# Kernel tuning notes

Measured on AMD Instinct MI355X. Metric: run time of the kernel, lower is better.

The kernel has to match this reference:

```python
import jax, jax.numpy as jnp
import numpy as np

E = 400000
N = 100000
B = 64
D = 128          # token_dim
H = 128          # hidden_dim
A = 2 * H        # action_dim


def setup_inputs() -> dict:
    key = jax.random.key(0)
    ks = jax.random.split(key, 12)
    inp = {
        "relation_tokens": jax.random.normal(ks[0], (E, D), jnp.float32),
        "node_tokens": jax.random.normal(ks[1], (N, D), jnp.float32),
        "edge_index": jax.random.randint(ks[2], (2, E), 0, N, jnp.int64 if jax.config.jax_enable_x64 else jnp.int32),
        "question_tokens": jax.random.normal(ks[3], (B, D), jnp.float32),
        "edge_batch": jax.random.randint(ks[4], (E,), 0, B, jnp.int64 if jax.config.jax_enable_x64 else jnp.int32),
        # learned params (xavier-like small init); stored as [in, out] for x @ W
        "W_rel": jax.random.normal(ks[5], (D, H), jnp.float32) * 0.05,
        "W_node": jax.random.normal(ks[6], (D, H), jnp.float32) * 0.05,
        "W_qgate": jax.random.normal(ks[7], (D, A), jnp.float32) * 0.05,
        "W_mlp1": jax.random.normal(ks[8], (A, A), jnp.float32) * 0.05,
        "b_mlp1": jnp.zeros((A,), jnp.float32),
        "W_mlp2": jax.random.normal(ks[9], (A, A), jnp.float32) * 0.05,
        "b_mlp2": jnp.zeros((A,), jnp.float32),
    }
    return inp


def reference(relation_tokens, node_tokens, edge_index, question_tokens, edge_batch,
              W_rel, W_node, W_qgate, W_mlp1, b_mlp1, W_mlp2, b_mlp2):
    # TrajectoryAgent.precompute_action_keys (dropout=0 -> identity)
    tail_nodes = edge_index[1]                       # [E]
    tail_tokens = node_tokens[tail_nodes]            # gather -> [E, D]
    q_tokens = question_tokens[edge_batch]           # gather -> [E, D]

    rel_key = relation_tokens @ W_rel                # [E, H]
    node_key = tail_tokens @ W_node                  # [E, H]
    q_gate = jax.nn.sigmoid(q_tokens @ W_qgate)      # [E, 2H]

    action_key = jnp.concatenate((rel_key, node_key), axis=-1) * q_gate  # [E, 2H]

    # action_mlp: Linear -> exact GELU -> Linear (torch nn.GELU default = erf)
    h = jax.nn.gelu(action_key @ W_mlp1 + b_mlp1, approximate=False)
    return h @ W_mlp2 + b_mlp2                       # [E, 2H]
```

## Files before the change

### kernel.cpp

```cpp
#include <hip/hip_runtime.h>

typedef __bf16 bf16;
typedef bf16 bf16x4 __attribute__((ext_vector_type(4)));
typedef bf16 bf16x8 __attribute__((ext_vector_type(8)));
typedef float f32x4 __attribute__((ext_vector_type(4)));

#define WS_PK1   0
#define WS_PK2   32768
#define WS_PK3   98304
#define WS_QG    163840

__global__ void prep_weights(const float* __restrict__ Wrel,
                             const float* __restrict__ Wnode,
                             const float* __restrict__ W1,
                             const float* __restrict__ W2,
                             bf16* __restrict__ ws) {
  int id = blockIdx.x * 256 + threadIdx.x;
  if (id < 32768) {
    int cg = id >> 13, rem = id & 8191;
    int kk = rem >> 11;
    int ai = (rem >> 9) & 3;
    int l  = (rem >> 3) & 63;
    int j  = rem & 7;
    int n  = (cg & 1) * 64 + ai * 16 + (l & 15);
    int k  = kk * 32 + (l >> 4) * 8 + j;
    const float* src = (cg >> 1) ? Wnode : Wrel;
    ws[WS_PK1 + id] = (bf16)src[k * 128 + n];
  } else if (id < 98304) {
    int t = id - 32768;
    int cg = t >> 14, rem = t & 16383;
    int kk = rem >> 11;
    int ai = (rem >> 9) & 3;
    int l  = (rem >> 3) & 63;
    int j  = rem & 7;
    int n  = cg * 64 + ai * 16 + (l & 15);
    int k  = kk * 32 + (l >> 4) * 8 + j;
    ws[WS_PK2 + t] = (bf16)W1[k * 256 + n];
  } else if (id < 163840) {
    int t = id - 98304;
    int cg = t >> 14, rem = t & 16383;
    int kk = rem >> 11;
    int ai = (rem >> 9) & 3;
    int l  = (rem >> 3) & 63;
    int j  = rem & 7;
    int n  = cg * 64 + ai * 16 + (l & 15);
    int k  = kk * 32 + (l >> 4) * 8 + j;
    ws[WS_PK3 + t] = (bf16)W2[k * 256 + n];
  }
}

__global__ void prep_qg(const float* __restrict__ question,
                        const float* __restrict__ Wq,
                        bf16* __restrict__ qg) {
  int b = blockIdx.x, c = threadIdx.x;
  float s = 0.f;
#pragma unroll 8
  for (int k = 0; k < 128; ++k) s += question[b * 128 + k] * Wq[k * 256 + c];
  qg[b * 256 + c] = (bf16)(1.f / (1.f + expf(-s)));
}

__device__ __forceinline__ float gelu_fast(float x) {
  float x2 = x * x;
  float p = fmaf(0.0356774081f, x2, 0.7978845608f);
  float y = p * x;
  float e = __expf(2.f * y);
  float r = __builtin_amdgcn_rcpf(e + 1.f);
  float th = 1.f - 2.f * r;
  return 0.5f * x * (1.f + th);
}

typedef __attribute__((address_space(1))) const void gq_t;
typedef __attribute__((address_space(3))) void lq_t;
#define GLD16(g, s) __builtin_amdgcn_global_load_lds((gq_t*)(g), (lq_t*)(s), 16, 0, 0)
#define SB() __builtin_amdgcn_sched_barrier(0xF)
#define WAIT_VM4()   { asm volatile("s_waitcnt vmcnt(4)" ::: "memory"); SB(); }
#define WAIT_VM0()   { asm volatile("s_waitcnt vmcnt(0)" ::: "memory"); SB(); }
#define WAIT_LGKM0() { asm volatile("s_waitcnt lgkmcnt(0)" ::: "memory"); SB(); }
#define BAR() __builtin_amdgcn_s_barrier()

__global__ __launch_bounds__(256, 2) void fused_main(
    const float* __restrict__ rel_tok,
    const float* __restrict__ node_tok,
    const int*   __restrict__ tail_idx,
    const int*   __restrict__ ebatch,
    const bf16*  __restrict__ pk1,
    const bf16*  __restrict__ pk2,
    const bf16*  __restrict__ pk3,
    const bf16*  __restrict__ qg,
    const float* __restrict__ b1,
    const float* __restrict__ b2,
    float* __restrict__ out)
{
  __shared__ char  s_buf[32768];
  __shared__ char  s_w[32768];
  __shared__ float s_bias[512];

  const int tid = threadIdx.x;
  const int cg  = tid >> 6;
  const int l   = tid & 63;
  const int lo  = l & 15;
  const int hi  = l >> 4;
  const int base = blockIdx.x * 64;
  const int h1  = cg >> 1;

  auto issue_step = [&](int s) {
    const bf16* g;
    if (s < 4)       g = pk1 + cg * 8192  + s * 2048;
    else if (s < 12) g = pk2 + cg * 16384 + (s - 4) * 2048;
    else             g = pk3 + cg * 16384 + (s - 12) * 2048;
    g += l * 8;
    char* d = s_w + (s & 1) * 16384 + cg * 4096;
#pragma unroll
    for (int ai = 0; ai < 4; ++ai) GLD16(g + ai * 512, d + ai * 1024);
  };

  int ebv[4];
#pragma unroll
  for (int bj = 0; bj < 4; ++bj) ebv[bj] = ebatch[base + bj * 16 + lo];
  bf16x4 gv[4][4];
#pragma unroll
  for (int bj = 0; bj < 4; ++bj)
#pragma unroll
    for (int ai = 0; ai < 4; ++ai)
      gv[bj][ai] = *(const bf16x4*)(qg + ebv[bj] * 256 + cg * 64 + ai * 16 + hi * 4);
  s_bias[tid]       = b1[tid];
  s_bias[256 + tid] = b2[tid];

  {
    const float4* g = (const float4*)rel_tok + (size_t)base * 32;
#pragma unroll
    for (int i = 0; i < 8; ++i) {
      int idx = tid + i * 256;
      int row = idx >> 5, c4 = idx & 31;
      float4 v = g[idx];
      bf16x4 b; b[0] = (bf16)v.x; b[1] = (bf16)v.y; b[2] = (bf16)v.z; b[3] = (bf16)v.w;
      int off = row * 256 + ((c4 * 8) ^ ((row & 15) << 4));
      *(bf16x4*)(s_buf + off) = b;
    }
#pragma unroll
    for (int i = 0; i < 8; ++i) {
      int idx = tid + i * 256;
      int row = idx >> 5, c4 = idx & 31;
      int tail = tail_idx[base + row];
      float4 v = ((const float4*)node_tok)[(size_t)tail * 32 + c4];
      bf16x4 b; b[0] = (bf16)v.x; b[1] = (bf16)v.y; b[2] = (bf16)v.z; b[3] = (bf16)v.w;
      int off = 16384 + row * 256 + ((c4 * 8) ^ ((row & 15) << 4));
      *(bf16x4*)(s_buf + off) = b;
    }
  }

  WAIT_VM0();
  issue_step(0);
  issue_step(1);
  WAIT_LGKM0();
  BAR();

  const f32x4 zero4 = {0.f, 0.f, 0.f, 0.f};
  const int wb = cg * 4096 + l * 16;

  f32x4 acc1[4][4];
#pragma unroll
  for (int ai = 0; ai < 4; ++ai)
#pragma unroll
    for (int bj = 0; bj < 4; ++bj) acc1[ai][bj] = zero4;

#pragma unroll
  for (int kk = 0; kk < 4; ++kk) {
    const int s = kk;
    WAIT_VM4();
    bf16x8 a[4];
#pragma unroll
    for (int ai = 0; ai < 4; ++ai)
      a[ai] = *(const bf16x8*)(s_w + (s & 1) * 16384 + wb + ai * 1024);
    WAIT_LGKM0();
    issue_step(s + 2);
    __builtin_amdgcn_s_setprio(1);
#pragma unroll
    for (int bj = 0; bj < 4; ++bj) {
      int e = bj * 16 + lo;
      bf16x8 b = *(const bf16x8*)(s_buf + h1 * 16384 + e * 256 +
                                  ((kk * 64 + hi * 16) ^ ((e & 15) << 4)));
#pragma unroll
      for (int ai = 0; ai < 4; ++ai)
        acc1[ai][bj] = __builtin_amdgcn_mfma_f32_16x16x32_bf16(a[ai], b, acc1[ai][bj], 0, 0, 0);
    }
    __builtin_amdgcn_s_setprio(0);
  }
  BAR();

#pragma unroll
  for (int bj = 0; bj < 4; ++bj) {
    int e = bj * 16 + lo;
#pragma unroll
    for (int ai = 0; ai < 4; ++ai) {
      int col0 = cg * 64 + ai * 16 + hi * 4;
      bf16x4 pk;
      pk[0] = (bf16)(acc1[ai][bj][0] * (float)gv[bj][ai][0]);
      pk[1] = (bf16)(acc1[ai][bj][1] * (float)gv[bj][ai][1]);
      pk[2] = (bf16)(acc1[ai][bj][2] * (float)gv[bj][ai][2]);
      pk[3] = (bf16)(acc1[ai][bj][3] * (float)gv[bj][ai][3]);
      int off = e * 512 + ((2 * col0) ^ ((e & 15) << 4));
      *(bf16x4*)(s_buf + off) = pk;
    }
  }
  WAIT_LGKM0();
  BAR();

  f32x4 acc2[4][4];
#pragma unroll
  for (int ai = 0; ai < 4; ++ai)
#pragma unroll
    for (int bj = 0; bj < 4; ++bj) acc2[ai][bj] = zero4;

#pragma unroll
  for (int kk = 0; kk < 8; ++kk) {
    const int s = 4 + kk;
    WAIT_VM4();
    bf16x8 a[4];
#pragma unroll
    for (int ai = 0; ai < 4; ++ai)
      a[ai] = *(const bf16x8*)(s_w + (s & 1) * 16384 + wb + ai * 1024);
    WAIT_LGKM0();
    issue_step(s + 2);
    __builtin_amdgcn_s_setprio(1);
#pragma unroll
    for (int bj = 0; bj < 4; ++bj) {
      int e = bj * 16 + lo;
      bf16x8 b = *(const bf16x8*)(s_buf + e * 512 +
                                  ((kk * 64 + hi * 16) ^ ((e & 15) << 4)));
#pragma unroll
      for (int ai = 0; ai < 4; ++ai)
        acc2[ai][bj] = __builtin_amdgcn_mfma_f32_16x16x32_bf16(a[ai], b, acc2[ai][bj], 0, 0, 0);
    }
    __builtin_amdgcn_s_setprio(0);
  }
  BAR();

#pragma unroll
  for (int bj = 0; bj < 4; ++bj) {
    int e = bj * 16 + lo;
#pragma unroll
    for (int ai = 0; ai < 4; ++ai) {
      int col0 = cg * 64 + ai * 16 + hi * 4;
      float4 bv = *(const float4*)(s_bias + col0);
      bf16x4 pk;
      pk[0] = (bf16)gelu_fast(acc2[ai][bj][0] + bv.x);
      pk[1] = (bf16)gelu_fast(acc2[ai][bj][1] + bv.y);
      pk[2] = (bf16)gelu_fast(acc2[ai][bj][2] + bv.z);
      pk[3] = (bf16)gelu_fast(acc2[ai][bj][3] + bv.w);
      int off = e * 512 + ((2 * col0) ^ ((e & 15) << 4));
      *(bf16x4*)(s_buf + off) = pk;
    }
  }
  WAIT_LGKM0();
  BAR();

  f32x4 acc3[4][4];
#pragma unroll
  for (int ai = 0; ai < 4; ++ai)
#pragma unroll
    for (int bj = 0; bj < 4; ++bj) acc3[ai][bj] = zero4;

#pragma unroll
  for (int kk = 0; kk < 8; ++kk) {
    const int s = 12 + kk;
    if (s < 19) { WAIT_VM4(); } else { WAIT_VM0(); }
    bf16x8 a[4];
#pragma unroll
    for (int ai = 0; ai < 4; ++ai)
      a[ai] = *(const bf16x8*)(s_w + (s & 1) * 16384 + wb + ai * 1024);
    WAIT_LGKM0();
    if (s + 2 <= 19) issue_step(s + 2);
    __builtin_amdgcn_s_setprio(1);
#pragma unroll
    for (int bj = 0; bj < 4; ++bj) {
      int e = bj * 16 + lo;
      bf16x8 b = *(const bf16x8*)(s_buf + e * 512 +
                                  ((kk * 64 + hi * 16) ^ ((e & 15) << 4)));
#pragma unroll
      for (int ai = 0; ai < 4; ++ai)
        acc3[ai][bj] = __builtin_amdgcn_mfma_f32_16x16x32_bf16(a[ai], b, acc3[ai][bj], 0, 0, 0);
    }
    __builtin_amdgcn_s_setprio(0);
  }

#pragma unroll
  for (int bj = 0; bj < 4; ++bj) {
    int e = bj * 16 + lo;
#pragma unroll
    for (int ai = 0; ai < 4; ++ai) {
      int col0 = cg * 64 + ai * 16 + hi * 4;
      float4 bv = *(const float4*)(s_bias + 256 + col0);
      float4 o;
      o.x = acc3[ai][bj][0] + bv.x;
      o.y = acc3[ai][bj][1] + bv.y;
      o.z = acc3[ai][bj][2] + bv.z;
      o.w = acc3[ai][bj][3] + bv.w;
      *(float4*)(out + (size_t)(base + e) * 256 + col0) = o;
    }
  }
}

extern "C" void kernel_launch(void* const* d_in, const int* in_sizes, int n_in,
                              void* d_out, int out_size, void* d_ws, size_t ws_size,
                              hipStream_t stream) {
  const float* rel    = (const float*)d_in[0];
  const float* node   = (const float*)d_in[1];
  const int*   eidx   = (const int*)d_in[2];
  const float* quest  = (const float*)d_in[3];
  const int*   ebat   = (const int*)d_in[4];
  const float* Wrel   = (const float*)d_in[5];
  const float* Wnode  = (const float*)d_in[6];
  const float* Wq     = (const float*)d_in[7];
  const float* W1     = (const float*)d_in[8];
  const float* bias1  = (const float*)d_in[9];
  const float* W2     = (const float*)d_in[10];
  const float* bias2  = (const float*)d_in[11];
  float* outp = (float*)d_out;
  bf16* ws = (bf16*)d_ws;

  const int E = in_sizes[4];

  prep_weights<<<640, 256, 0, stream>>>(Wrel, Wnode, W1, W2, ws);
  prep_qg<<<64, 256, 0, stream>>>(quest, Wq, ws + WS_QG);
  fused_main<<<E / 64, 256, 0, stream>>>(
      rel, node, eidx + E, ebat,
      ws + WS_PK1, ws + WS_PK2, ws + WS_PK3, ws + WS_QG,
      bias1, bias2, outp);
}
```

Before: 281.8 us.

## Stream weights through a 4-slot sub-step LDS ring to fit three blocks per CU

Weight tiles are now fetched in 4KB sub-steps into a 4-slot LDS ring with three loads in flight, instead of two 16KB double-buffered steps. Waits move to per-sub-step vmcnt checks, and the B operand fragments are loaded once per k-step before the per-ai MFMA groups. This halves the weight LDS buffer, so launch bounds can request three blocks per CU, aiming for more latency hiding and occupancy. The cost is finer-grained waits and more issue overhead per sub-step. Register pressure under the tighter launch bound may also cause spills.

```diff
diff --git a/kernel.cpp b/kernel.cpp
--- a/kernel.cpp
+++ b/kernel.cpp
@@ -72,13 +72,17 @@
 typedef __attribute__((address_space(1))) const void gq_t;
 typedef __attribute__((address_space(3))) void lq_t;
 #define GLD16(g, s) __builtin_amdgcn_global_load_lds((gq_t*)(g), (lq_t*)(s), 16, 0, 0)
-#define SB() __builtin_amdgcn_sched_barrier(0xF)
-#define WAIT_VM4()   { asm volatile("s_waitcnt vmcnt(4)" ::: "memory"); SB(); }
-#define WAIT_VM0()   { asm volatile("s_waitcnt vmcnt(0)" ::: "memory"); SB(); }
-#define WAIT_LGKM0() { asm volatile("s_waitcnt lgkmcnt(0)" ::: "memory"); SB(); }
+#define SBF() __builtin_amdgcn_sched_barrier(0xF)
+#define SB7() __builtin_amdgcn_sched_barrier(0x7)
+#define WAIT_VM0()   { asm volatile("s_waitcnt vmcnt(0)" ::: "memory"); SBF(); }
+#define WAIT_LGKM0() { asm volatile("s_waitcnt lgkmcnt(0)" ::: "memory"); SBF(); }
+#define VMWAIT(u)    { if ((u) <= 77)      { asm volatile("s_waitcnt vmcnt(2)" ::: "memory"); } \
+                       else if ((u) == 78) { asm volatile("s_waitcnt vmcnt(1)" ::: "memory"); } \
+                       else                { asm volatile("s_waitcnt vmcnt(0)" ::: "memory"); } \
+                       SBF(); }
 #define BAR() __builtin_amdgcn_s_barrier()
 
-__global__ __launch_bounds__(256, 2) void fused_main(
+__global__ __launch_bounds__(256, 3) void fused_main(
     const float* __restrict__ rel_tok,
     const float* __restrict__ node_tok,
     const int*   __restrict__ tail_idx,
@@ -92,7 +96,7 @@
     float* __restrict__ out)
 {
   __shared__ char  s_buf[32768];
-  __shared__ char  s_w[32768];
+  __shared__ char  s_w[16384];
   __shared__ float s_bias[512];
 
   const int tid = threadIdx.x;
@@ -103,15 +107,12 @@
   const int base = blockIdx.x * 64;
   const int h1  = cg >> 1;
 
-  auto issue_step = [&](int s) {
+  auto issue_sub = [&](int u) {
     const bf16* g;
-    if (s < 4)       g = pk1 + cg * 8192  + s * 2048;
-    else if (s < 12) g = pk2 + cg * 16384 + (s - 4) * 2048;
-    else             g = pk3 + cg * 16384 + (s - 12) * 2048;
-    g += l * 8;
-    char* d = s_w + (s & 1) * 16384 + cg * 4096;
-#pragma unroll
-    for (int ai = 0; ai < 4; ++ai) GLD16(g + ai * 512, d + ai * 1024);
+    if (u < 16)      g = pk1 + cg * 8192  + u * 512;
+    else if (u < 48) g = pk2 + cg * 16384 + (u - 16) * 512;
+    else             g = pk3 + cg * 16384 + (u - 48) * 512;
+    GLD16(g + l * 8, s_w + (u & 3) * 4096 + cg * 1024 + l * 16);
   };
 
   int ebv[4];
@@ -150,13 +151,14 @@
   }
 
   WAIT_VM0();
-  issue_step(0);
-  issue_step(1);
+  issue_sub(0);
+  issue_sub(1);
+  issue_sub(2);
   WAIT_LGKM0();
   BAR();
 
   const f32x4 zero4 = {0.f, 0.f, 0.f, 0.f};
-  const int wb = cg * 4096 + l * 16;
+  const int wrd = cg * 1024 + l * 16;
 
   f32x4 acc1[4][4];
 #pragma unroll
@@ -166,25 +168,26 @@
 
 #pragma unroll
   for (int kk = 0; kk < 4; ++kk) {
-    const int s = kk;
-    WAIT_VM4();
-    bf16x8 a[4];
-#pragma unroll
-    for (int ai = 0; ai < 4; ++ai)
-      a[ai] = *(const bf16x8*)(s_w + (s & 1) * 16384 + wb + ai * 1024);
-    WAIT_LGKM0();
-    issue_step(s + 2);
-    __builtin_amdgcn_s_setprio(1);
+    bf16x8 bf[4];
 #pragma unroll
     for (int bj = 0; bj < 4; ++bj) {
       int e = bj * 16 + lo;
-      bf16x8 b = *(const bf16x8*)(s_buf + h1 * 16384 + e * 256 +
-                                  ((kk * 64 + hi * 16) ^ ((e & 15) << 4)));
-#pragma unroll
-      for (int ai = 0; ai < 4; ++ai)
-        acc1[ai][bj] = __builtin_amdgcn_mfma_f32_16x16x32_bf16(a[ai], b, acc1[ai][bj], 0, 0, 0);
-    }
-    __builtin_amdgcn_s_setprio(0);
+      bf[bj] = *(const bf16x8*)(s_buf + h1 * 16384 + e * 256 +
+                                ((kk * 64 + hi * 16) ^ ((e & 15) << 4)));
+    }
+#pragma unroll
+    for (int ai = 0; ai < 4; ++ai) {
+      const int u = kk * 4 + ai;
+      VMWAIT(u);
+      bf16x8 a = *(const bf16x8*)(s_w + (u & 3) * 4096 + wrd);
+      __builtin_amdgcn_s_setprio(1);
+#pragma unroll
+      for (int bj = 0; bj < 4; ++bj)
+        acc1[ai][bj] = __builtin_amdgcn_mfma_f32_16x16x32_bf16(a, bf[bj], acc1[ai][bj], 0, 0, 0);
+      __builtin_amdgcn_s_setprio(0);
+      SB7();
+      issue_sub(u + 3);
+    }
   }
   BAR();
 
@@ -214,25 +217,26 @@
 
 #pragma unroll
   for (int kk = 0; kk < 8; ++kk) {
-    const int s = 4 + kk;
-    WAIT_VM4();
-    bf16x8 a[4];
-#pragma unroll
-    for (int ai = 0; ai < 4; ++ai)
-      a[ai] = *(const bf16x8*)(s_w + (s & 1) * 16384 + wb + ai * 1024);
-    WAIT_LGKM0();
-    issue_step(s + 2);
-    __builtin_amdgcn_s_setprio(1);
+    bf16x8 bf[4];
 #pragma unroll
     for (int bj = 0; bj < 4; ++bj) {
       int e = bj * 16 + lo;
-      bf16x8 b = *(const bf16x8*)(s_buf + e * 512 +
-                                  ((kk * 64 + hi * 16) ^ ((e & 15) << 4)));
-#pragma unroll
-      for (int ai = 0; ai < 4; ++ai)
-        acc2[ai][bj] = __builtin_amdgcn_mfma_f32_16x16x32_bf16(a[ai], b, acc2[ai][bj], 0, 0, 0);
-    }
-    __builtin_amdgcn_s_setprio(0);
+      bf[bj] = *(const bf16x8*)(s_buf + e * 512 +
+                                ((kk * 64 + hi * 16) ^ ((e & 15) << 4)));
+    }
+#pragma unroll
+    for (int ai = 0; ai < 4; ++ai) {
+      const int u = 16 + kk * 4 + ai;
+      VMWAIT(u);
+      bf16x8 a = *(const bf16x8*)(s_w + (u & 3) * 4096 + wrd);
+      __builtin_amdgcn_s_setprio(1);
+#pragma unroll
+      for (int bj = 0; bj < 4; ++bj)
+        acc2[ai][bj] = __builtin_amdgcn_mfma_f32_16x16x32_bf16(a, bf[bj], acc2[ai][bj], 0, 0, 0);
+      __builtin_amdgcn_s_setprio(0);
+      SB7();
+      issue_sub(u + 3);
+    }
   }
   BAR();
 
@@ -263,25 +267,25 @@
 
 #pragma unroll
   for (int kk = 0; kk < 8; ++kk) {
-    const int s = 12 + kk;
-    if (s < 19) { WAIT_VM4(); } else { WAIT_VM0(); }
-    bf16x8 a[4];
-#pragma unroll
-    for (int ai = 0; ai < 4; ++ai)
-      a[ai] = *(const bf16x8*)(s_w + (s & 1) * 16384 + wb + ai * 1024);
-    WAIT_LGKM0();
-    if (s + 2 <= 19) issue_step(s + 2);
-    __builtin_amdgcn_s_setprio(1);
+    bf16x8 bf[4];
 #pragma unroll
     for (int bj = 0; bj < 4; ++bj) {
       int e = bj * 16 + lo;
-      bf16x8 b = *(const bf16x8*)(s_buf + e * 512 +
-                                  ((kk * 64 + hi * 16) ^ ((e & 15) << 4)));
-#pragma unroll
-      for (int ai = 0; ai < 4; ++ai)
-        acc3[ai][bj] = __builtin_amdgcn_mfma_f32_16x16x32_bf16(a[ai], b, acc3[ai][bj], 0, 0, 0);
-    }
-    __builtin_amdgcn_s_setprio(0);
+      bf[bj] = *(const bf16x8*)(s_buf + e * 512 +
+                                ((kk * 64 + hi * 16) ^ ((e & 15) << 4)));
+    }
+#pragma unroll
+    for (int ai = 0; ai < 4; ++ai) {
+      const int u = 48 + kk * 4 + ai;
+      VMWAIT(u);
+      bf16x8 a = *(const bf16x8*)(s_w + (u & 3) * 4096 + wrd);
+      __builtin_amdgcn_s_setprio(1);
+#pragma unroll
+      for (int bj = 0; bj < 4; ++bj)
+        acc3[ai][bj] = __builtin_amdgcn_mfma_f32_16x16x32_bf16(a, bf[bj], acc3[ai][bj], 0, 0, 0);
+      __builtin_amdgcn_s_setprio(0);
+      if (u + 3 < 80) { SB7(); issue_sub(u + 3); }
+    }
   }
 
 #pragma unroll
```

Measured after the change: 285.4 us. No clear change (+1.3%).

## Make fused kernel persistent and prefetch next tile's inputs during GEMMs

Applied to the files above, without the earlier changes.

The fused kernel now runs as a persistent grid of 512 blocks, each looping over 64-edge tiles with a stride of the grid size. Tail indices and batch ids for the next tile are loaded during the first GEMM. Relation rows, gathered node rows and q-gate values are loaded into registers during the last GEMM and written to LDS after the output store. This hides the input-gather latency behind MFMA work and removes per-block launch and prologue cost, at the price of more register pressure (rv/nv/gv2 arrays), which could spill or hurt occupancy at 2 blocks per CU.

```diff
diff --git a/kernel.cpp b/kernel.cpp
--- a/kernel.cpp
+++ b/kernel.cpp
@@ -72,10 +72,9 @@
 typedef __attribute__((address_space(1))) const void gq_t;
 typedef __attribute__((address_space(3))) void lq_t;
 #define GLD16(g, s) __builtin_amdgcn_global_load_lds((gq_t*)(g), (lq_t*)(s), 16, 0, 0)
-#define SB() __builtin_amdgcn_sched_barrier(0xF)
-#define WAIT_VM4()   { asm volatile("s_waitcnt vmcnt(4)" ::: "memory"); SB(); }
-#define WAIT_VM0()   { asm volatile("s_waitcnt vmcnt(0)" ::: "memory"); SB(); }
-#define WAIT_LGKM0() { asm volatile("s_waitcnt lgkmcnt(0)" ::: "memory"); SB(); }
+#define SBF() __builtin_amdgcn_sched_barrier(0xF)
+#define WAIT_VM(n)   { asm volatile("s_waitcnt vmcnt(" #n ")" ::: "memory"); SBF(); }
+#define WAIT_LGKM0() { asm volatile("s_waitcnt lgkmcnt(0)" ::: "memory"); SBF(); }
 #define BAR() __builtin_amdgcn_s_barrier()
 
 __global__ __launch_bounds__(256, 2) void fused_main(
@@ -89,7 +88,8 @@
     const bf16*  __restrict__ qg,
     const float* __restrict__ b1,
     const float* __restrict__ b2,
-    float* __restrict__ out)
+    float* __restrict__ out,
+    int ntiles, int G)
 {
   __shared__ char  s_buf[32768];
   __shared__ char  s_w[32768];
@@ -100,8 +100,8 @@
   const int l   = tid & 63;
   const int lo  = l & 15;
   const int hi  = l >> 4;
-  const int base = blockIdx.x * 64;
   const int h1  = cg >> 1;
+  const int c4s = tid & 31;
 
   auto issue_step = [&](int s) {
     const bf16* g;
@@ -114,190 +114,241 @@
     for (int ai = 0; ai < 4; ++ai) GLD16(g + ai * 512, d + ai * 1024);
   };
 
-  int ebv[4];
-#pragma unroll
-  for (int bj = 0; bj < 4; ++bj) ebv[bj] = ebatch[base + bj * 16 + lo];
-  bf16x4 gv[4][4];
-#pragma unroll
-  for (int bj = 0; bj < 4; ++bj)
-#pragma unroll
-    for (int ai = 0; ai < 4; ++ai)
-      gv[bj][ai] = *(const bf16x4*)(qg + ebv[bj] * 256 + cg * 64 + ai * 16 + hi * 4);
   s_bias[tid]       = b1[tid];
   s_bias[256 + tid] = b2[tid];
 
+  const int t0 = blockIdx.x;
+  bf16x4 gv[4][4];
   {
-    const float4* g = (const float4*)rel_tok + (size_t)base * 32;
+    int ebv[4];
+#pragma unroll
+    for (int bj = 0; bj < 4; ++bj) ebv[bj] = ebatch[t0 * 64 + bj * 16 + lo];
+#pragma unroll
+    for (int bj = 0; bj < 4; ++bj)
+#pragma unroll
+      for (int ai = 0; ai < 4; ++ai)
+        gv[bj][ai] = *(const bf16x4*)(qg + ebv[bj] * 256 + cg * 64 + ai * 16 + hi * 4);
+    const float4* g = (const float4*)rel_tok + (size_t)t0 * 2048;
 #pragma unroll
     for (int i = 0; i < 8; ++i) {
-      int idx = tid + i * 256;
-      int row = idx >> 5, c4 = idx & 31;
-      float4 v = g[idx];
+      int row = (tid >> 5) + 8 * i;
+      float4 v = g[tid + i * 256];
       bf16x4 b; b[0] = (bf16)v.x; b[1] = (bf16)v.y; b[2] = (bf16)v.z; b[3] = (bf16)v.w;
-      int off = row * 256 + ((c4 * 8) ^ ((row & 15) << 4));
+      int off = row * 256 + ((c4s * 8) ^ ((row & 15) << 4));
       *(bf16x4*)(s_buf + off) = b;
     }
 #pragma unroll
     for (int i = 0; i < 8; ++i) {
-      int idx = tid + i * 256;
-      int row = idx >> 5, c4 = idx & 31;
-      int tail = tail_idx[base + row];
-      float4 v = ((const float4*)node_tok)[(size_t)tail * 32 + c4];
+      int row = (tid >> 5) + 8 * i;
+      int tail = tail_idx[t0 * 64 + row];
+      float4 v = ((const float4*)node_tok)[(size_t)tail * 32 + c4s];
       bf16x4 b; b[0] = (bf16)v.x; b[1] = (bf16)v.y; b[2] = (bf16)v.z; b[3] = (bf16)v.w;
-      int off = 16384 + row * 256 + ((c4 * 8) ^ ((row & 15) << 4));
+      int off = 16384 + row * 256 + ((c4s * 8) ^ ((row & 15) << 4));
       *(bf16x4*)(s_buf + off) = b;
     }
   }
 
-  WAIT_VM0();
-  issue_step(0);
-  issue_step(1);
-  WAIT_LGKM0();
-  BAR();
-
   const f32x4 zero4 = {0.f, 0.f, 0.f, 0.f};
-  const int wb = cg * 4096 + l * 16;
-
-  f32x4 acc1[4][4];
-#pragma unroll
-  for (int ai = 0; ai < 4; ++ai)
-#pragma unroll
-    for (int bj = 0; bj < 4; ++bj) acc1[ai][bj] = zero4;
-
-#pragma unroll
-  for (int kk = 0; kk < 4; ++kk) {
-    const int s = kk;
-    WAIT_VM4();
-    bf16x8 a[4];
+  const int wrd = cg * 4096 + l * 16;
+
+  for (int t = t0; t < ntiles; t += G) {
+    const int base = t * 64;
+    int tn = t + G; if (tn >= ntiles) tn = t;
+
+    WAIT_VM(0);
+    issue_step(0);
+    issue_step(1);
+    WAIT_LGKM0();
+    BAR();
+
+    int t2l[8], eb2v[4];
+    bf16x4 gv2[4][4];
+
+    f32x4 acc1[4][4];
 #pragma unroll
     for (int ai = 0; ai < 4; ++ai)
-      a[ai] = *(const bf16x8*)(s_w + (s & 1) * 16384 + wb + ai * 1024);
-    WAIT_LGKM0();
-    issue_step(s + 2);
-    __builtin_amdgcn_s_setprio(1);
+#pragma unroll
+      for (int bj = 0; bj < 4; ++bj) acc1[ai][bj] = zero4;
+
+#pragma unroll
+    for (int kk = 0; kk < 4; ++kk) {
+      if (kk == 0)      { WAIT_VM(4); }
+      else if (kk < 3)  { WAIT_VM(16); }
+      else              { WAIT_VM(4); }
+      bf16x8 a[4];
+#pragma unroll
+      for (int ai = 0; ai < 4; ++ai)
+        a[ai] = *(const bf16x8*)(s_w + (kk & 1) * 16384 + wrd + ai * 1024);
+      WAIT_LGKM0();
+      issue_step(kk + 2);
+      if (kk == 0) {
+        SBF();
+#pragma unroll
+        for (int i = 0; i < 8; ++i) t2l[i] = tail_idx[tn * 64 + (tid >> 5) + 8 * i];
+#pragma unroll
+        for (int bj = 0; bj < 4; ++bj) eb2v[bj] = ebatch[tn * 64 + bj * 16 + lo];
+        SBF();
+      }
+      __builtin_amdgcn_s_setprio(1);
+#pragma unroll
+      for (int bj = 0; bj < 4; ++bj) {
+        int e = bj * 16 + lo;
+        bf16x8 b = *(const bf16x8*)(s_buf + h1 * 16384 + e * 256 +
+                                    ((kk * 64 + hi * 16) ^ ((e & 15) << 4)));
+#pragma unroll
+        for (int ai = 0; ai < 4; ++ai)
+          acc1[ai][bj] = __builtin_amdgcn_mfma_f32_16x16x32_bf16(a[ai], b, acc1[ai][bj], 0, 0, 0);
+      }
+      __builtin_amdgcn_s_setprio(0);
+    }
+    BAR();
+
 #pragma unroll
     for (int bj = 0; bj < 4; ++bj) {
       int e = bj * 16 + lo;
-      bf16x8 b = *(const bf16x8*)(s_buf + h1 * 16384 + e * 256 +
-                                  ((kk * 64 + hi * 16) ^ ((e & 15) << 4)));
+#pragma unroll
+      for (int ai = 0; ai < 4; ++ai) {
+        int col0 = cg * 64 + ai * 16 + hi * 4;
+        bf16x4 pk;
+        pk[0] = (bf16)(acc1[ai][bj][0] * (float)gv[bj][ai][0]);
+        pk[1] = (bf16)(acc1[ai][bj][1] * (float)gv[bj][ai][1]);
+        pk[2] = (bf16)(acc1[ai][bj][2] * (float)gv[bj][ai][2]);
+        pk[3] = (bf16)(acc1[ai][bj][3] * (float)gv[bj][ai][3]);
+        int off = e * 512 + ((2 * col0) ^ ((e & 15) << 4));
+        *(bf16x4*)(s_buf + off) = pk;
+      }
+    }
+    WAIT_LGKM0();
+    BAR();
+
+    f32x4 acc2[4][4];
+#pragma unroll
+    for (int ai = 0; ai < 4; ++ai)
+#pragma unroll
+      for (int bj = 0; bj < 4; ++bj) acc2[ai][bj] = zero4;
+
+#pragma unroll
+    for (int kk = 0; kk < 8; ++kk) {
+      const int s = 4 + kk;
+      WAIT_VM(4);
+      bf16x8 a[4];
 #pragma unroll
       for (int ai = 0; ai < 4; ++ai)
-        acc1[ai][bj] = __builtin_amdgcn_mfma_f32_16x16x32_bf16(a[ai], b, acc1[ai][bj], 0, 0, 0);
-    }
-    __builtin_amdgcn_s_setprio(0);
-  }
-  BAR();
-
-#pragma unroll
-  for (int bj = 0; bj < 4; ++bj) {
-    int e = bj * 16 + lo;
-#pragma unroll
-    for (int ai = 0; ai < 4; ++ai) {
-      int col0 = cg * 64 + ai * 16 + hi * 4;
-      bf16x4 pk;
-      pk[0] = (bf16)(acc1[ai][bj][0] * (float)gv[bj][ai][0]);
-      pk[1] = (bf16)(acc1[ai][bj][1] * (float)gv[bj][ai][1]);
-      pk[2] = (bf16)(acc1[ai][bj][2] * (float)gv[bj][ai][2]);
-      pk[3] = (bf16)(acc1[ai][bj][3] * (float)gv[bj][ai][3]);
-      int off = e * 512 + ((2 * col0) ^ ((e & 15) << 4));
-      *(bf16x4*)(s_buf + off) = pk;
-    }
-  }
-  WAIT_LGKM0();
-  BAR();
-
-  f32x4 acc2[4][4];
-#pragma unroll
-  for (int ai = 0; ai < 4; ++ai)
-#pragma unroll
-    for (int bj = 0; bj < 4; ++bj) acc2[ai][bj] = zero4;
-
-#pragma unroll
-  for (int kk = 0; kk < 8; ++kk) {
-    const int s = 4 + kk;
-    WAIT_VM4();
-    bf16x8 a[4];
-#pragma unroll
-    for (int ai = 0; ai < 4; ++ai)
-      a[ai] = *(const bf16x8*)(s_w + (s & 1) * 16384 + wb + ai * 1024);
-    WAIT_LGKM0();
-    issue_step(s + 2);
-    __builtin_amdgcn_s_setprio(1);
+        a[ai] = *(const bf16x8*)(s_w + (s & 1) * 16384 + wrd + ai * 1024);
+      WAIT_LGKM0();
+      issue_step(s + 2);
+      __builtin_amdgcn_s_setprio(1);
+#pragma unroll
+      for (int bj = 0; bj < 4; ++bj) {
+        int e = bj * 16 + lo;
+        bf16x8 b = *(const bf16x8*)(s_buf + e * 512 +
+                                    ((kk * 64 + hi * 16) ^ ((e & 15) << 4)));
+#pragma unroll
+        for (int ai = 0; ai < 4; ++ai)
+          acc2[ai][bj] = __builtin_amdgcn_mfma_f32_16x16x32_bf16(a[ai], b, acc2[ai][bj], 0, 0, 0);
+      }
+      __builtin_amdgcn_s_setprio(0);
+    }
+    BAR();
+
 #pragma unroll
     for (int bj = 0; bj < 4; ++bj) {
       int e = bj * 16 + lo;
-      bf16x8 b = *(const bf16x8*)(s_buf + e * 512 +
-                                  ((kk * 64 + hi * 16) ^ ((e & 15) << 4)));
+#pragma unroll
+      for (int ai = 0; ai < 4; ++ai) {
+        int col0 = cg * 64 + ai * 16 + hi * 4;
+        float4 bv = *(const float4*)(s_bias + col0);
+        bf16x4 pk;
+        pk[0] = (bf16)gelu_fast(acc2[ai][bj][0] + bv.x);
+        pk[1] = (bf16)gelu_fast(acc2[ai][bj][1] + bv.y);
+        pk[2] = (bf16)gelu_fast(acc2[ai][bj][2] + bv.z);
+        pk[3] = (bf16)gelu_fast(acc2[ai][bj][3] + bv.w);
+        int off = e * 512 + ((2 * col0) ^ ((e & 15) << 4));
+        *(bf16x4*)(s_buf + off) = pk;
+      }
+    }
+    WAIT_LGKM0();
+    BAR();
+
+    f32x4 acc3[4][4];
+#pragma unroll
+    for (int ai = 0; ai < 4; ++ai)
+#pragma unroll
+      for (int bj = 0; bj < 4; ++bj) acc3[ai][bj] = zero4;
+
+    float4 rv[8], nv[8];
+
+#pragma unroll
+    for (int kk = 0; kk < 8; ++kk) {
+      const int s = 12 + kk;
+      if (s < 19) { WAIT_VM(4); } else { WAIT_VM(0); }
+      bf16x8 a[4];
 #pragma unroll
       for (int ai = 0; ai < 4; ++ai)
-        acc2[ai][bj] = __builtin_amdgcn_mfma_f32_16x16x32_bf16(a[ai], b, acc2[ai][bj], 0, 0, 0);
-    }
-    __builtin_amdgcn_s_setprio(0);
-  }
-  BAR();
-
-#pragma unroll
-  for (int bj = 0; bj < 4; ++bj) {
-    int e = bj * 16 + lo;
-#pragma unroll
-    for (int ai = 0; ai < 4; ++ai) {
-      int col0 = cg * 64 + ai * 16 + hi * 4;
-      float4 bv = *(const float4*)(s_bias + col0);
-      bf16x4 pk;
-      pk[0] = (bf16)gelu_fast(acc2[ai][bj][0] + bv.x);
-      pk[1] = (bf16)gelu_fast(acc2[ai][bj][1] + bv.y);
-      pk[2] = (bf16)gelu_fast(acc2[ai][bj][2] + bv.z);
-      pk[3] = (bf16)gelu_fast(acc2[ai][bj][3] + bv.w);
-      int off = e * 512 + ((2 * col0) ^ ((e & 15) << 4));
-      *(bf16x4*)(s_buf + off) = pk;
-    }
-  }
-  WAIT_LGKM0();
-  BAR();
-
-  f32x4 acc3[4][4];
-#pragma unroll
-  for (int ai = 0; ai < 4; ++ai)
-#pragma unroll
-    for (int bj = 0; bj < 4; ++bj) acc3[ai][bj] = zero4;
-
-#pragma unroll
-  for (int kk = 0; kk < 8; ++kk) {
-    const int s = 12 + kk;
-    if (s < 19) { WAIT_VM4(); } else { WAIT_VM0(); }
-    bf16x8 a[4];
-#pragma unroll
-    for (int ai = 0; ai < 4; ++ai)
-      a[ai] = *(const bf16x8*)(s_w + (s & 1) * 16384 + wb + ai * 1024);
-    WAIT_LGKM0();
-    if (s + 2 <= 19) issue_step(s + 2);
-    __builtin_amdgcn_s_setprio(1);
+        a[ai] = *(const bf16x8*)(s_w + (s & 1) * 16384 + wrd + ai * 1024);
+      WAIT_LGKM0();
+      if (s + 2 <= 19) issue_step(s + 2);
+      if (s == 19) {
+        SBF();
+        const float4* gr = (const float4*)rel_tok + (size_t)tn * 2048;
+#pragma unroll
+        for (int i = 0; i < 8; ++i) rv[i] = gr[tid + i * 256];
+#pragma unroll
+        for (int i = 0; i < 8; ++i)
+          nv[i] = ((const float4*)node_tok)[(size_t)t2l[i] * 32 + c4s];
+#pragma unroll
+        for (int bj = 0; bj < 4; ++bj)
+#pragma unroll
+          for (int ai = 0; ai < 4; ++ai)
+            gv2[bj][ai] = *(const bf16x4*)(qg + eb2v[bj] * 256 + cg * 64 + ai * 16 + hi * 4);
+        SBF();
+      }
+      __builtin_amdgcn_s_setprio(1);
+#pragma unroll
+      for (int bj = 0; bj < 4; ++bj) {
+        int e = bj * 16 + lo;
+        bf16x8 b = *(const bf16x8*)(s_buf + e * 512 +
+                                    ((kk * 64 + hi * 16) ^ ((e & 15) << 4)));
+#pragma unroll
+        for (int ai = 0; ai < 4; ++ai)
+          acc3[ai][bj] = __builtin_amdgcn_mfma_f32_16x16x32_bf16(a[ai], b, acc3[ai][bj], 0, 0, 0);
+      }
+      __builtin_amdgcn_s_setprio(0);
+    }
+    BAR();
+
 #pragma unroll
     for (int bj = 0; bj < 4; ++bj) {
       int e = bj * 16 + lo;
-      bf16x8 b = *(const bf16x8*)(s_buf + e * 512 +
-                                  ((kk * 64 + hi * 16) ^ ((e & 15) << 4)));
-#pragma unroll
-      for (int ai = 0; ai < 4; ++ai)
-        acc3[ai][bj] = __builtin_amdgcn_mfma_f32_16x16x32_bf16(a[ai], b, acc3[ai][bj], 0, 0, 0);
-    }
-    __builtin_amdgcn_s_setprio(0);
-  }
-
-#pragma unroll
-  for (int bj = 0; bj < 4; ++bj) {
-    int e = bj * 16 + lo;
-#pragma unroll
-    for (int ai = 0; ai < 4; ++ai) {
-      int col0 = cg * 64 + ai * 16 + hi * 4;
-      float4 bv = *(const float4*)(s_bias + 256 + col0);
-      float4 o;
-      o.x = acc3[ai][bj][0] + bv.x;
-      o.y = acc3[ai][bj][1] + bv.y;
-      o.z = acc3[ai][bj][2] + bv.z;
-      o.w = acc3[ai][bj][3] + bv.w;
-      *(float4*)(out + (size_t)(base + e) * 256 + col0) = o;
-    }
+#pragma unroll
+      for (int ai = 0; ai < 4; ++ai) {
+        int col0 = cg * 64 + ai * 16 + hi * 4;
+        float4 bv = *(const float4*)(s_bias + 256 + col0);
+        float4 o;
+        o.x = acc3[ai][bj][0] + bv.x;
+        o.y = acc3[ai][bj][1] + bv.y;
+        o.z = acc3[ai][bj][2] + bv.z;
+        o.w = acc3[ai][bj][3] + bv.w;
+        *(float4*)(out + (size_t)(base + e) * 256 + col0) = o;
+      }
+    }
+    SBF();
+    WAIT_VM(16);
+#pragma unroll
+    for (int i = 0; i < 8; ++i) {
+      int row = (tid >> 5) + 8 * i;
+      float4 v = rv[i];
+      bf16x4 b; b[0] = (bf16)v.x; b[1] = (bf16)v.y; b[2] = (bf16)v.z; b[3] = (bf16)v.w;
+      int off = row * 256 + ((c4s * 8) ^ ((row & 15) << 4));
+      *(bf16x4*)(s_buf + off) = b;
+      float4 u = nv[i];
+      bf16x4 c; c[0] = (bf16)u.x; c[1] = (bf16)u.y; c[2] = (bf16)u.z; c[3] = (bf16)u.w;
+      *(bf16x4*)(s_buf + 16384 + off) = c;
+    }
+#pragma unroll
+    for (int bj = 0; bj < 4; ++bj)
+#pragma unroll
+      for (int ai = 0; ai < 4; ++ai) gv[bj][ai] = gv2[bj][ai];
   }
 }
 
@@ -320,11 +371,13 @@
   bf16* ws = (bf16*)d_ws;
 
   const int E = in_sizes[4];
+  const int ntiles = E / 64;
+  const int G = 512;
 
   prep_weights<<<640, 256, 0, stream>>>(Wrel, Wnode, W1, W2, ws);
   prep_qg<<<64, 256, 0, stream>>>(quest, Wq, ws + WS_QG);
-  fused_main<<<E / 64, 256, 0, stream>>>(
+  fused_main<<<G, 256, 0, stream>>>(
       rel, node, eidx + E, ebat,
       ws + WS_PK1, ws + WS_PK2, ws + WS_PK3, ws + WS_QG,
-      bias1, bias2, outp);
-}
+      bias1, bias2, outp, ntiles, G);
+}
```

Result: slower. 557.4 us (+97.8%).
